# Optimization experiments

Measured on AMD Instinct MI355X. Metric: run time of the kernel, lower is better.

## Reference

```python
import jax, jax.numpy as jnp
import numpy as np

B, N, K = 16, 8192, 16
H1, H3 = 512, 64
EPS = 1e-5


def _bn(x, g, b):
    # BatchNorm1d training-mode math: normalize per-channel (last axis) over all other axes.
    ax = tuple(range(x.ndim - 1))
    m = x.mean(ax, keepdims=True)
    v = x.var(ax, keepdims=True)  # biased variance, as in torch BN forward
    return (x - m) * jax.lax.rsqrt(v + EPS) * g + b


def _gather(h, idx):
    # h: [b,n,f], idx: [b,n,k] -> [b,n,k,f] per-batch neighbor gather
    return jax.vmap(lambda hb, ib: hb[ib])(h, idx)


def _forward(data, knn, e1_w, e1_b, e1_g, e1_be,
             gc1_w, gc1_b, g1_g, g1_be, gc2_w, gc2_b, g2_g, g2_be,
             e2_w, e2_b, e2_g, e2_be,
             d1_w, d1_b, d1_g, d1_be, d2_w, d2_b, d2_g, d2_be):
    b, n, _ = data.shape
    # local covariance features
    neigh = _gather(data, knn)                       # [b,n,K,3]
    cen = neigh - neigh.mean(axis=2, keepdims=True)
    cov = jnp.einsum('bnki,bnkj->bnij', cen, cen) / (K - 1)
    x = jnp.concatenate([data, cov.reshape(b, n, 9)], axis=-1)  # [b,n,12]
    # e_layers1: Linear(12,h3) + BN + ReLU
    x = jax.nn.relu(_bn(x @ e1_w + e1_b, e1_g, e1_be))
    # GCNConv over uniform-degree kNN graph with self loop: (h_i + sum_j h_j)/(K+1)
    deg = float(K + 1)
    h = x @ gc1_w
    h = (h + _gather(h, knn).sum(axis=2)) / deg + gc1_b
    x = jax.nn.relu(_bn(h, g1_g, g1_be))
    h = x @ gc2_w
    h = (h + _gather(h, knn).sum(axis=2)) / deg + gc2_b
    x = jax.nn.relu(_bn(h, g2_g, g2_be))             # [b,n,h1]
    # AdaptiveMaxPool1d(1) over nodes
    x = x.max(axis=1, keepdims=True)                 # [b,1,h1]
    # e_layers2: Linear(h1,h1) + BN + ReLU
    x = jax.nn.relu(_bn(x @ e2_w + e2_b, e2_g, e2_be))
    # decode: folding grid
    nx_ = int(1 + (n * 120 / 60) ** 0.5)
    ny_ = int(1 + (n * 60 / 120) ** 0.5)
    xg = jnp.linspace(1.0, 120.0, nx_)
    yg = jnp.linspace(1.0, 60.0, ny_)
    grid = jnp.stack(jnp.meshgrid(xg, yg, indexing='ij'), axis=-1).reshape(-1, 2)[:n]
    kfeat = jnp.broadcast_to(x, (b, n, x.shape[-1]))  # codeword repeated per node
    y = jnp.broadcast_to(grid[None], (b, n, 2))
    z = jnp.concatenate([kfeat, y], axis=-1)          # [b,n,h1+2]
    z = jax.nn.relu(_bn(z @ d1_w + d1_b, d1_g, d1_be))
    z = jnp.concatenate([kfeat, z], axis=-1)          # [b,n,h1+3]
    z = jax.nn.relu(_bn(z @ d2_w + d2_b, d2_g, d2_be))
    return z                                          # [b,n,3]


def setup_inputs() -> dict:
    key = jax.random.key(0)
    ks = jax.random.split(key, 8)

    def lin(k, i, o):
        s = 1.0 / np.sqrt(i)
        return jax.random.uniform(k, (i, o), jnp.float32, -s, s)

    ones = lambda c: jnp.ones((c,), jnp.float32)
    zeros = lambda c: jnp.zeros((c,), jnp.float32)
    return {
        'data': jax.random.normal(ks[0], (B, N, 3), jnp.float32),
        'knn': jax.random.randint(ks[1], (B, N, K), 0, N),
        'e1_w': lin(ks[2], 12, H3), 'e1_b': zeros(H3), 'e1_g': ones(H3), 'e1_be': zeros(H3),
        'gc1_w': lin(ks[3], H3, 2 * H3), 'gc1_b': zeros(2 * H3), 'g1_g': ones(2 * H3), 'g1_be': zeros(2 * H3),
        'gc2_w': lin(ks[4], 2 * H3, H1), 'gc2_b': zeros(H1), 'g2_g': ones(H1), 'g2_be': zeros(H1),
        'e2_w': lin(ks[5], H1, H1), 'e2_b': zeros(H1), 'e2_g': ones(H1), 'e2_be': zeros(H1),
        'd1_w': lin(ks[6], H1 + 2, 3), 'd1_b': zeros(3), 'd1_g': ones(3), 'd1_be': zeros(3),
        'd2_w': lin(ks[7], H1 + 3, 3), 'd2_b': zeros(3), 'd2_g': ones(3), 'd2_be': zeros(3),
    }


def reference(data, knn, e1_w, e1_b, e1_g, e1_be,
              gc1_w, gc1_b, g1_g, g1_be, gc2_w, gc2_b, g2_g, g2_be,
              e2_w, e2_b, e2_g, e2_be,
              d1_w, d1_b, d1_g, d1_be, d2_w, d2_b, d2_g, d2_be):
    return _forward(data, knn, e1_w, e1_b, e1_g, e1_be,
                    gc1_w, gc1_b, g1_g, g1_be, gc2_w, gc2_b, g2_g, g2_be,
                    e2_w, e2_b, e2_g, e2_be,
                    d1_w, d1_b, d1_g, d1_be, d2_w, d2_b, d2_g, d2_be)
```

## Files before the change

### kernel.cpp

```cpp
#include <hip/hip_runtime.h>
#include <hip/hip_fp16.h>
#include <stdint.h>

#define BATCH 16
#define NPTS  8192
#define KNN   16
#define NROWS (BATCH*NPTS)
#define EPSBN 1e-5f
#define DEGINV (1.0f/17.0f)

typedef _Float16 f16x8 __attribute__((ext_vector_type(8)));
typedef float    f32x4 __attribute__((ext_vector_type(4)));

__device__ __forceinline__ unsigned short f2hu(float f) {
    union { _Float16 h; unsigned short u; } cv;
    cv.h = (_Float16)f;
    return cv.u;
}
__device__ __forceinline__ float hu2f(unsigned short u) {
    union { unsigned short u; _Float16 h; } cv;
    cv.u = u;
    return (float)cv.h;
}
__device__ __forceinline__ unsigned fenc(float f) {
    unsigned u = __float_as_uint(f);
    return (int)u >= 0 ? (u | 0x80000000u) : ~u;
}
__device__ __forceinline__ float fdec(unsigned k) {
    return (k & 0x80000000u) ? __uint_as_float(k & 0x7FFFFFFFu) : __uint_as_float(~k);
}

#define SZ_S1    0
#define SZ_S2P   128
#define SZ_S3P   16512
#define SZ_S4    82048
#define SZ_C1    83072
#define SZ_GN    83080
#define SZ_D2    83088
#define SZ_SCSH1 83096
#define SZ_SCSH2 83224
#define SZ_TOT   83480

__global__ __launch_bounds__(256) void k_prep(
    const float* __restrict__ gc1w, const float* __restrict__ gc2w,
    const float* __restrict__ d1w, const float* __restrict__ d1b,
    unsigned short* __restrict__ W1T, unsigned short* __restrict__ W2T,
    float* __restrict__ gn, float* __restrict__ statszone, unsigned* __restrict__ mm)
{
    int t = blockIdx.x * 256 + threadIdx.x;
    int NT_ = gridDim.x * 256;
    for (int i = t; i < 65536; i += NT_) {
        int c = i >> 7, k = i & 127;
        W2T[i] = f2hu(gc2w[k * 512 + c]);
    }
    for (int i = t; i < 8192; i += NT_) {
        int c = i >> 6, k = i & 63;
        W1T[i] = f2hu(gc1w[k * 128 + c]);
    }
    for (int i = t; i < SZ_TOT; i += NT_) statszone[i] = 0.f;
    for (int i = t; i < 8192; i += NT_) mm[i] = 0u;
    for (int i = t; i < 8192; i += NT_) mm[8192 + i] = 0xFFFFFFFFu;
    for (int n = t; n < 8192; n += NT_) {
        int ix = n / 65, iy = n % 65;
        float gx = 1.f + ix * (119.f / 128.f);
        float gy = 1.f + iy * (59.f / 64.f);
        #pragma unroll
        for (int j = 0; j < 3; j++)
            gn[n * 3 + j] = gx * d1w[512 * 3 + j] + gy * d1w[513 * 3 + j] + d1b[j];
    }
}

__global__ __launch_bounds__(256) void k_cov_e1(
    const float* __restrict__ data, const int* __restrict__ knn,
    const float* __restrict__ e1w, const float* __restrict__ e1b,
    unsigned short* __restrict__ a1)
{
    __shared__ float w[12 * 64];
    __shared__ float bias[64];
    int tid = threadIdx.x;
    for (int i = tid; i < 768; i += 256) w[i] = e1w[i];
    if (tid < 64) bias[tid] = e1b[tid];
    __syncthreads();

    int gid = blockIdx.x * 256 + tid;
    int b = gid >> 13;
    const float* db = data + (size_t)b * NPTS * 3;
    const int4* k4 = (const int4*)knn + gid * 4;

    float sx = 0, sy = 0, sz = 0, Sxx = 0, Sxy = 0, Sxz = 0, Syy = 0, Syz = 0, Szz = 0;
    #pragma unroll
    for (int jj = 0; jj < 4; jj++) {
        int4 q = k4[jj];
        int id[4] = {q.x, q.y, q.z, q.w};
        #pragma unroll
        for (int u = 0; u < 4; u++) {
            const float* p = db + (size_t)id[u] * 3;
            float x = p[0], y = p[1], z = p[2];
            sx += x; sy += y; sz += z;
            Sxx += x * x; Sxy += x * y; Sxz += x * z;
            Syy += y * y; Syz += y * z; Szz += z * z;
        }
    }
    float mx = sx * (1.f / 16.f), my = sy * (1.f / 16.f), mz = sz * (1.f / 16.f);
    const float inv15 = 1.f / 15.f;
    float x12[12];
    x12[0] = data[(size_t)gid * 3 + 0];
    x12[1] = data[(size_t)gid * 3 + 1];
    x12[2] = data[(size_t)gid * 3 + 2];
    x12[3] = (Sxx - 16.f * mx * mx) * inv15;
    x12[4] = (Sxy - 16.f * mx * my) * inv15;
    x12[5] = (Sxz - 16.f * mx * mz) * inv15;
    x12[6] = x12[4];
    x12[7] = (Syy - 16.f * my * my) * inv15;
    x12[8] = (Syz - 16.f * my * mz) * inv15;
    x12[9] = x12[5];
    x12[10] = x12[8];
    x12[11] = (Szz - 16.f * mz * mz) * inv15;

    unsigned short* arow = a1 + (size_t)gid * 64;
    for (int c0 = 0; c0 < 64; c0 += 8) {
        float v8[8];
        #pragma unroll
        for (int u = 0; u < 8; u++) {
            int c = c0 + u;
            float acc = bias[c];
            #pragma unroll
            for (int i = 0; i < 12; i++) acc += x12[i] * w[i * 64 + c];
            v8[u] = acc;
        }
        uint4 o;
        o.x = f2hu(v8[0]) | ((unsigned)f2hu(v8[1]) << 16);
        o.y = f2hu(v8[2]) | ((unsigned)f2hu(v8[3]) << 16);
        o.z = f2hu(v8[4]) | ((unsigned)f2hu(v8[5]) << 16);
        o.w = f2hu(v8[6]) | ((unsigned)f2hu(v8[7]) << 16);
        *(uint4*)(arow + c0) = o;
    }
}

__global__ __launch_bounds__(256) void k_reduce_a1(
    const unsigned short* __restrict__ a1, float* __restrict__ stats1)
{
    int tid = threadIdx.x;
    int c = tid & 63, rq = tid >> 6;
    float s = 0.f, q = 0.f;
    for (int row = blockIdx.x * 4 + rq; row < NROWS; row += gridDim.x * 4) {
        float v = hu2f(a1[(size_t)row * 64 + c]);
        s += v; q += v * v;
    }
    __shared__ float red[2][256];
    red[0][tid] = s; red[1][tid] = q;
    __syncthreads();
    if (tid < 64) {
        s = red[0][tid] + red[0][tid + 64] + red[0][tid + 128] + red[0][tid + 192];
        q = red[1][tid] + red[1][tid + 64] + red[1][tid + 128] + red[1][tid + 192];
        atomicAdd(stats1 + tid, s);
        atomicAdd(stats1 + 64 + tid, q);
    }
}

template <int C, int NPARTS>
__global__ __launch_bounds__(256) void k_bncoef(
    const float* __restrict__ statsIn,
    const float* __restrict__ gamma, const float* __restrict__ beta,
    float* __restrict__ scsh)
{
    int ch = threadIdx.x;
    if (ch < C) {
        float s = 0.f, q = 0.f;
        for (int p = 0; p < NPARTS; p++) {
            s += statsIn[p * 2 * C + ch];
            q += statsIn[p * 2 * C + C + ch];
        }
        float m = s * (1.f / NROWS);
        float var = fmaxf(q * (1.f / NROWS) - m * m, 0.f);
        float sc = gamma[ch] * rsqrtf(var + EPSBN);
        scsh[ch] = sc;
        scsh[C + ch] = beta[ch] - m * sc;
    }
}

template <int CIN>
__global__ __launch_bounds__(256) void k_gather16(
    const unsigned short* __restrict__ ain, const int* __restrict__ knn,
    const float* __restrict__ scsh, unsigned short* __restrict__ S)
{
    constexpr int GPR = CIN / 8;
    constexpr int R = 256 / GPR;
    constexpr int BPB = NPTS / R;

    __shared__ int nidx[R * KNN];

    int tid = threadIdx.x;
    int blk = blockIdx.x;
    int xcd = blk & 7;
    int idx = blk >> 3;
    int batch = xcd + 8 * (idx / BPB);
    int within = idx % BPB;
    int node0 = batch * NPTS + within * R;

    if (tid < R * KNN / 4) {
        const int4* ksrc = (const int4*)(knn + (size_t)node0 * KNN);
        ((int4*)nidx)[tid] = ksrc[tid];
    }
    __syncthreads();

    int t = tid & (GPR - 1);
    int r = tid / GPR;
    int col8 = t * 8;
    float sc8[8], sh8[8];
    #pragma unroll
    for (int j = 0; j < 8; j++) { sc8[j] = scsh[col8 + j]; sh8[j] = scsh[CIN + col8 + j]; }

    int row = node0 + r;
    const unsigned short* abase = ain + (size_t)batch * NPTS * CIN;

    float acc8[8];
    {
        uint4 v = *(const uint4*)(ain + (size_t)row * CIN + col8);
        unsigned wds[4] = {v.x, v.y, v.z, v.w};
        #pragma unroll
        for (int j = 0; j < 4; j++) {
            acc8[2*j]   = fmaxf(hu2f((unsigned short)(wds[j] & 0xFFFF)) * sc8[2*j]   + sh8[2*j],   0.f);
            acc8[2*j+1] = fmaxf(hu2f((unsigned short)(wds[j] >> 16))    * sc8[2*j+1] + sh8[2*j+1], 0.f);
        }
    }
    #pragma unroll
    for (int jn = 0; jn < KNN; jn++) {
        int src = nidx[r * KNN + jn];
        uint4 v = *(const uint4*)(abase + (size_t)src * CIN + col8);
        unsigned wds[4] = {v.x, v.y, v.z, v.w};
        #pragma unroll
        for (int j = 0; j < 4; j++) {
            acc8[2*j]   += fmaxf(hu2f((unsigned short)(wds[j] & 0xFFFF)) * sc8[2*j]   + sh8[2*j],   0.f);
            acc8[2*j+1] += fmaxf(hu2f((unsigned short)(wds[j] >> 16))    * sc8[2*j+1] + sh8[2*j+1], 0.f);
        }
    }
    uint4 o;
    o.x = f2hu(acc8[0]) | ((unsigned)f2hu(acc8[1]) << 16);
    o.y = f2hu(acc8[2]) | ((unsigned)f2hu(acc8[3]) << 16);
    o.z = f2hu(acc8[4]) | ((unsigned)f2hu(acc8[5]) << 16);
    o.w = f2hu(acc8[6]) | ((unsigned)f2hu(acc8[7]) << 16);
    *(uint4*)(S + (size_t)row * CIN + col8) = o;
}

template <int CIN, int COUT, int NSPLIT, bool STORE>
__global__ __launch_bounds__(256) void k_gemm(
    const unsigned short* __restrict__ S, const unsigned short* __restrict__ WT,
    const float* __restrict__ bias,
    unsigned short* __restrict__ aout, float* __restrict__ statsOut, unsigned* __restrict__ mm)
{
    constexpr int KC = CIN / 32;
    constexpr int MT = 128;
    constexpr int SST = CIN + 8;
    constexpr int CPB = COUT / NSPLIT;
    constexpr int CPW = CPB / 4;
    constexpr int NT = CPW / 16;

    __shared__ alignas(16) unsigned short sA[MT * SST];

    int tid = threadIdx.x;
    int blk = blockIdx.x;
    int xcd = blk & 7;
    int rest = blk >> 3;
    int nq = rest % NSPLIT;
    int mseq = rest / NSPLIT;
    int phase = mseq >> 6;
    int within = mseq & 63;
    int batch = xcd + 8 * phase;
    int node0 = batch * NPTS + within * MT;
    int cbase = nq * CPB;
    int pout = batch * 4 + (within >> 4);

    {
        constexpr int TOT = MT * CIN / 8;
        const uint4* src = (const uint4*)(S + (size_t)node0 * CIN);
        #pragma unroll
        for (int i = tid; i < TOT; i += 256) {
            int row = i / (CIN / 8);
            int col8 = (i % (CIN / 8)) * 8;
            *(uint4*)&sA[row * SST + col8] = src[i];
        }
    }
    __syncthreads();

    int lane = tid & 63, wv = tid >> 6;
    int n15 = lane & 15, qd = lane >> 4;
    int c0 = cbase + wv * CPW;

    f16x8 wf[KC][NT];
    float bz[NT];
    #pragma unroll
    for (int nt = 0; nt < NT; nt++) {
        int c = c0 + nt * 16 + n15;
        bz[nt] = bias[c];
        #pragma unroll
        for (int kc = 0; kc < KC; kc++)
            wf[kc][nt] = *(const f16x8*)(WT + (size_t)c * CIN + kc * 32 + qd * 8);
    }
    float sacc[NT], qacc[NT], mxa[NT], mna[NT];
    #pragma unroll
    for (int nt = 0; nt < NT; nt++) {
        sacc[nt] = 0.f; qacc[nt] = 0.f; mxa[nt] = -3.4e38f; mna[nt] = 3.4e38f;
    }

    #pragma unroll
    for (int mt = 0; mt < MT / 16; mt++) {
        f16x8 af[KC];
        #pragma unroll
        for (int kc = 0; kc < KC; kc++)
            af[kc] = *(const f16x8*)&sA[(mt * 16 + n15) * SST + kc * 32 + qd * 8];

        f32x4 acc[NT];
        #pragma unroll
        for (int nt = 0; nt < NT; nt++) acc[nt] = (f32x4)(0.f);
        #pragma unroll
        for (int kc = 0; kc < KC; kc++)
            #pragma unroll
            for (int nt = 0; nt < NT; nt++)
                acc[nt] = __builtin_amdgcn_mfma_f32_16x16x32_f16(af[kc], wf[kc][nt], acc[nt], 0, 0, 0);

        #pragma unroll
        for (int nt = 0; nt < NT; nt++) {
            int c = c0 + nt * 16 + n15;
            #pragma unroll
            for (int r = 0; r < 4; r++) {
                float a = acc[nt][r];
                sacc[nt] += a;
                qacc[nt] = fmaf(a, a, qacc[nt]);
                if (!STORE) {
                    mxa[nt] = fmaxf(mxa[nt], a);
                    mna[nt] = fminf(mna[nt], a);
                }
                if (STORE) {
                    float v = a * DEGINV + bz[nt];
                    int node = node0 + mt * 16 + qd * 4 + r;
                    aout[(size_t)node * COUT + c] = f2hu(v);
                }
            }
        }
    }

    #pragma unroll
    for (int nt = 0; nt < NT; nt++) {
        int c = c0 + nt * 16 + n15;
        float S_ = sacc[nt], Q_ = qacc[nt];
        S_ += __shfl_xor(S_, 16); S_ += __shfl_xor(S_, 32);
        Q_ += __shfl_xor(Q_, 16); Q_ += __shfl_xor(Q_, 32);
        if (!STORE) {
            float mx = mxa[nt], mn = mna[nt];
            mx = fmaxf(mx, __shfl_xor(mx, 16)); mx = fmaxf(mx, __shfl_xor(mx, 32));
            mn = fminf(mn, __shfl_xor(mn, 16)); mn = fminf(mn, __shfl_xor(mn, 32));
            if (lane < 16) {
                atomicMax(mm + batch * COUT + c, fenc(mx * DEGINV + bz[nt]));
                atomicMin(mm + BATCH * COUT + batch * COUT + c, fenc(mn * DEGINV + bz[nt]));
            }
        }
        if (lane < 16) {
            float b = bz[nt];
            float s = DEGINV * S_ + (float)MT * b;
            float q = DEGINV * DEGINV * Q_ + 2.f * DEGINV * b * S_ + (float)MT * b * b;
            atomicAdd(statsOut + (size_t)pout * 2 * COUT + c, s);
            atomicAdd(statsOut + (size_t)pout * 2 * COUT + COUT + c, q);
        }
    }
}

__global__ __launch_bounds__(256) void k_e2(
    const float* __restrict__ stats3p, const unsigned* __restrict__ mm,
    const float* __restrict__ g2g, const float* __restrict__ g2be,
    const float* __restrict__ e2w, const float* __restrict__ e2b,
    float* __restrict__ a4, float* __restrict__ stats4)
{
    __shared__ float pooled[512];
    int b = blockIdx.x, tid = threadIdx.x;
    for (int c = tid; c < 512; c += 256) {
        float s = 0.f, qq = 0.f;
        for (int p = 0; p < 64; p++) {
            s += stats3p[p * 1024 + c];
            qq += stats3p[p * 1024 + 512 + c];
        }
        float m = s * (1.f / NROWS);
        float var = fmaxf(qq * (1.f / NROWS) - m * m, 0.f);
        float sc = g2g[c] * rsqrtf(var + EPSBN);
        float sh = g2be[c] - m * sc;
        float amax = fdec(mm[b * 512 + c]);
        float amin = fdec(mm[8192 + b * 512 + c]);
        pooled[c] = fmaxf(fmaxf(sc * amax + sh, 0.f), fmaxf(sc * amin + sh, 0.f));
    }
    __syncthreads();
    int ca = tid, cb = tid + 256;
    float acc1 = e2b[ca], acc2 = e2b[cb];
    for (int f = 0; f < 512; f++) {
        float pv = pooled[f];
        acc1 += pv * e2w[f * 512 + ca];
        acc2 += pv * e2w[f * 512 + cb];
    }
    a4[b * 512 + ca] = acc1; a4[b * 512 + cb] = acc2;
    atomicAdd(stats4 + ca, acc1); atomicAdd(stats4 + 512 + ca, acc1 * acc1);
    atomicAdd(stats4 + cb, acc2); atomicAdd(stats4 + 512 + cb, acc2 * acc2);
}

__global__ __launch_bounds__(256) void k_code(
    const float* __restrict__ a4, const float* __restrict__ stats4,
    const float* __restrict__ e2g, const float* __restrict__ e2be,
    const float* __restrict__ d1w, const float* __restrict__ d2w,
    const float* __restrict__ gn,
    float* __restrict__ c1, float* __restrict__ c2,
    float* __restrict__ c1stats, float* __restrict__ gnstats)
{
    int b = blockIdx.x, tid = threadIdx.x;
    int lane = tid & 63, wv = tid >> 6;
    float p1[3] = {0, 0, 0}, p2[3] = {0, 0, 0};
    for (int c = tid; c < 512; c += 256) {
        float s = stats4[c], qq = stats4[512 + c];
        float m = s * (1.f / 16.f);
        float var = fmaxf(qq * (1.f / 16.f) - m * m, 0.f);
        float sc = e2g[c] * rsqrtf(var + EPSBN);
        float sh = e2be[c] - m * sc;
        float cv = fmaxf(sc * a4[b * 512 + c] + sh, 0.f);
        #pragma unroll
        for (int j = 0; j < 3; j++) {
            p1[j] += cv * d1w[c * 3 + j];
            p2[j] += cv * d2w[c * 3 + j];
        }
    }
    __shared__ float red[4][6];
    #pragma unroll
    for (int j = 0; j < 3; j++)
        for (int off = 32; off; off >>= 1) {
            p1[j] += __shfl_xor(p1[j], off);
            p2[j] += __shfl_xor(p2[j], off);
        }
    if (lane == 0) {
        #pragma unroll
        for (int j = 0; j < 3; j++) { red[wv][j] = p1[j]; red[wv][3 + j] = p2[j]; }
    }
    __syncthreads();
    if (tid < 3) {
        float v = red[0][tid] + red[1][tid] + red[2][tid] + red[3][tid];
        c1[b * 3 + tid] = v;
        atomicAdd(c1stats + tid, v);
        atomicAdd(c1stats + 3 + tid, v * v);
    } else if (tid < 6) {
        int j = tid - 3;
        float v = red[0][tid] + red[1][tid] + red[2][tid] + red[3][tid];
        c2[b * 3 + j] = v;
    }
    if (blockIdx.x == 0) {
        float g1[3] = {0, 0, 0}, g2s[3] = {0, 0, 0};
        for (int n = tid; n < NPTS; n += 256) {
            #pragma unroll
            for (int j = 0; j < 3; j++) {
                float g = gn[n * 3 + j];
                g1[j] += g; g2s[j] += g * g;
            }
        }
        #pragma unroll
        for (int j = 0; j < 3; j++)
            for (int off = 32; off; off >>= 1) {
                g1[j] += __shfl_xor(g1[j], off);
                g2s[j] += __shfl_xor(g2s[j], off);
            }
        __shared__ float redg[4][6];
        if (lane == 0) {
            #pragma unroll
            for (int j = 0; j < 3; j++) { redg[wv][j] = g1[j]; redg[wv][3 + j] = g2s[j]; }
        }
        __syncthreads();
        if (tid < 6)
            gnstats[tid] = redg[0][tid] + redg[1][tid] + redg[2][tid] + redg[3][tid];
    }
}

__device__ __forceinline__ void d1_coefs(
    const float* c1stats, const float* gnstats,
    const float* d1g, const float* d1be, float* scd, float* shd)
{
    #pragma unroll
    for (int j = 0; j < 3; j++) {
        float mc = c1stats[j] * (1.f / 16.f), qc = c1stats[3 + j] * (1.f / 16.f);
        float mg = gnstats[j] * (1.f / 8192.f), qg = gnstats[3 + j] * (1.f / 8192.f);
        float m = mc + mg;
        float var = fmaxf((qc - mc * mc) + (qg - mg * mg), 0.f);
        float sc = d1g[j] * rsqrtf(var + EPSBN);
        scd[j] = sc;
        shd[j] = d1be[j] - m * sc;
    }
}

__global__ __launch_bounds__(256) void k_d2stats(
    const float* __restrict__ c1, const float* __restrict__ c2, const float* __restrict__ gn,
    const float* __restrict__ c1stats, const float* __restrict__ gnstats,
    const float* __restrict__ d1g, const float* __restrict__ d1be,
    const float* __restrict__ d2w, const float* __restrict__ d2b,
    float* __restrict__ statsd2)
{
    int gid = blockIdx.x * 256 + threadIdx.x;
    int b = gid >> 13, n = gid & 8191;
    int lane = threadIdx.x & 63, wv = threadIdx.x >> 6;
    float scd[3], shd[3];
    d1_coefs(c1stats, gnstats, d1g, d1be, scd, shd);
    float z3[3];
    #pragma unroll
    for (int j = 0; j < 3; j++)
        z3[j] = fmaxf(scd[j] * (c1[b * 3 + j] + gn[n * 3 + j]) + shd[j], 0.f);
    float vals[6];
    #pragma unroll
    for (int u = 0; u < 3; u++) {
        float a = c2[b * 3 + u]
                + z3[0] * d2w[512 * 3 + u]
                + z3[1] * d2w[513 * 3 + u]
                + z3[2] * d2w[514 * 3 + u]
                + d2b[u];
        vals[u] = a; vals[3 + u] = a * a;
    }
    #pragma unroll
    for (int j = 0; j < 6; j++)
        for (int off = 32; off; off >>= 1) vals[j] += __shfl_xor(vals[j], off);
    __shared__ float red[4][6];
    if (lane == 0) {
        #pragma unroll
        for (int j = 0; j < 6; j++) red[wv][j] = vals[j];
    }
    __syncthreads();
    if (threadIdx.x < 6)
        atomicAdd(statsd2 + threadIdx.x,
                  red[0][threadIdx.x] + red[1][threadIdx.x] + red[2][threadIdx.x] + red[3][threadIdx.x]);
}

__global__ __launch_bounds__(256) void k_out(
    const float* __restrict__ c1, const float* __restrict__ c2, const float* __restrict__ gn,
    const float* __restrict__ c1stats, const float* __restrict__ gnstats,
    const float* __restrict__ statsd2,
    const float* __restrict__ d1g, const float* __restrict__ d1be,
    const float* __restrict__ d2w, const float* __restrict__ d2b,
    const float* __restrict__ d2g, const float* __restrict__ d2be,
    float* __restrict__ out)
{
    int gid = blockIdx.x * 256 + threadIdx.x;
    int b = gid >> 13, n = gid & 8191;
    float scd[3], shd[3];
    d1_coefs(c1stats, gnstats, d1g, d1be, scd, shd);
    float z3[3];
    #pragma unroll
    for (int j = 0; j < 3; j++)
        z3[j] = fmaxf(scd[j] * (c1[b * 3 + j] + gn[n * 3 + j]) + shd[j], 0.f);
    #pragma unroll
    for (int u = 0; u < 3; u++) {
        float a = c2[b * 3 + u]
                + z3[0] * d2w[512 * 3 + u]
                + z3[1] * d2w[513 * 3 + u]
                + z3[2] * d2w[514 * 3 + u]
                + d2b[u];
        float m2 = statsd2[u] * (1.f / (float)NROWS);
        float v2 = fmaxf(statsd2[3 + u] * (1.f / (float)NROWS) - m2 * m2, 0.f);
        float sc = d2g[u] * rsqrtf(v2 + EPSBN);
        float sh = d2be[u] - m2 * sc;
        out[(size_t)gid * 3 + u] = fmaxf(sc * a + sh, 0.f);
    }
}

extern "C" void kernel_launch(void* const* d_in, const int* in_sizes, int n_in,
                              void* d_out, int out_size, void* d_ws, size_t ws_size,
                              hipStream_t stream)
{
    (void)in_sizes; (void)n_in; (void)out_size; (void)ws_size;
    const float* data = (const float*)d_in[0];
    const int*   knn  = (const int*)d_in[1];
    const float* e1w = (const float*)d_in[2],  *e1b = (const float*)d_in[3];
    const float* e1g = (const float*)d_in[4],  *e1be = (const float*)d_in[5];
    const float* gc1w = (const float*)d_in[6], *gc1b = (const float*)d_in[7];
    const float* g1g = (const float*)d_in[8],  *g1be = (const float*)d_in[9];
    const float* gc2w = (const float*)d_in[10], *gc2b = (const float*)d_in[11];
    const float* g2g = (const float*)d_in[12], *g2be = (const float*)d_in[13];
    const float* e2w = (const float*)d_in[14], *e2b = (const float*)d_in[15];
    const float* e2g = (const float*)d_in[16], *e2be = (const float*)d_in[17];
    const float* d1w = (const float*)d_in[18], *d1b = (const float*)d_in[19];
    const float* d1g = (const float*)d_in[20], *d1be = (const float*)d_in[21];
    const float* d2w = (const float*)d_in[22], *d2b = (const float*)d_in[23];
    const float* d2g = (const float*)d_in[24], *d2be = (const float*)d_in[25];

    char* p = (char*)d_ws;
    auto alloc = [&](size_t bytes) -> void* {
        void* r = (void*)p;
        p += (bytes + 255) & ~(size_t)255;
        return r;
    };
    unsigned short* a1  = (unsigned short*)alloc((size_t)NROWS * 64 * 2);
    unsigned short* a2h = (unsigned short*)alloc((size_t)NROWS * 128 * 2);
    unsigned short* s1  = (unsigned short*)alloc((size_t)NROWS * 64 * 2);
    unsigned short* s2  = (unsigned short*)alloc((size_t)NROWS * 128 * 2);
    unsigned short* W1T = (unsigned short*)alloc(8192 * 2);
    unsigned short* W2T = (unsigned short*)alloc(65536 * 2);
    float* statszone = (float*)alloc(SZ_TOT * 4);
    float* stats1  = statszone + SZ_S1;
    float* stats2p = statszone + SZ_S2P;
    float* stats3p = statszone + SZ_S3P;
    float* stats4  = statszone + SZ_S4;
    float* c1stats = statszone + SZ_C1;
    float* gnstats = statszone + SZ_GN;
    float* statsd2 = statszone + SZ_D2;
    float* scsh1   = statszone + SZ_SCSH1;
    float* scsh2   = statszone + SZ_SCSH2;
    unsigned* mm = (unsigned*)alloc(16384 * 4);
    float* a4 = (float*)alloc(16 * 512 * 4);
    float* c1 = (float*)alloc(64 * 4);
    float* c2 = (float*)alloc(64 * 4);
    float* gn = (float*)alloc(8192 * 3 * 4);

    k_prep<<<64, 256, 0, stream>>>(gc1w, gc2w, d1w, d1b, W1T, W2T, gn, statszone, mm);
    k_cov_e1<<<512, 256, 0, stream>>>(data, knn, e1w, e1b, a1);
    k_reduce_a1<<<256, 256, 0, stream>>>(a1, stats1);
    k_bncoef<64, 1><<<1, 256, 0, stream>>>(stats1, e1g, e1be, scsh1);
    k_gather16<64><<<NROWS / 32, 256, 0, stream>>>(a1, knn, scsh1, s1);
    k_gemm<64, 128, 1, true><<<1024, 256, 0, stream>>>(s1, W1T, gc1b, a2h, stats2p, nullptr);
    k_bncoef<128, 64><<<1, 256, 0, stream>>>(stats2p, g1g, g1be, scsh2);
    k_gather16<128><<<NROWS / 16, 256, 0, stream>>>(a2h, knn, scsh2, s2);
    k_gemm<128, 512, 4, false><<<4096, 256, 0, stream>>>(s2, W2T, gc2b, nullptr, stats3p, mm);
    k_e2<<<16, 256, 0, stream>>>(stats3p, mm, g2g, g2be, e2w, e2b, a4, stats4);
    k_code<<<16, 256, 0, stream>>>(a4, stats4, e2g, e2be, d1w, d2w, gn, c1, c2, c1stats, gnstats);
    k_d2stats<<<512, 256, 0, stream>>>(c1, c2, gn, c1stats, gnstats, d1g, d1be, d2w, d2b, statsd2);
    k_out<<<512, 256, 0, stream>>>(c1, c2, gn, c1stats, gnstats, statsd2,
                                   d1g, d1be, d2w, d2b, d2g, d2be, (float*)d_out);
}
```

Measured before the change: 334.9 us.

## Fuse BN1 stats into cov kernel and process two rows per gather thread

Computes the first BatchNorm's sum and sum-of-squares inside k_cov_e1 via wavefront shuffle reductions and atomics into 8 partial slots, which removes the separate k_reduce_a1 pass that re-read a1. The gather kernels now handle two node rows per thread, halving the grid size and putting two independent neighbor loads in flight per iteration. In exchange, the cov kernel does more work, issues more atomics to a small set of addresses, and the gather threads use more registers.

```diff
diff --git a/kernel.cpp b/kernel.cpp
--- a/kernel.cpp
+++ b/kernel.cpp
@@ -31,15 +31,15 @@
 }
 
 #define SZ_S1    0
-#define SZ_S2P   128
-#define SZ_S3P   16512
-#define SZ_S4    82048
-#define SZ_C1    83072
-#define SZ_GN    83080
-#define SZ_D2    83088
-#define SZ_SCSH1 83096
-#define SZ_SCSH2 83224
-#define SZ_TOT   83480
+#define SZ_S2P   1024
+#define SZ_S3P   17408
+#define SZ_S4    82944
+#define SZ_C1    83968
+#define SZ_GN    83976
+#define SZ_D2    83984
+#define SZ_SCSH1 83992
+#define SZ_SCSH2 84120
+#define SZ_TOT   84376
 
 __global__ __launch_bounds__(256) void k_prep(
     const float* __restrict__ gc1w, const float* __restrict__ gc2w,
@@ -73,7 +73,7 @@
 __global__ __launch_bounds__(256) void k_cov_e1(
     const float* __restrict__ data, const int* __restrict__ knn,
     const float* __restrict__ e1w, const float* __restrict__ e1b,
-    unsigned short* __restrict__ a1)
+    unsigned short* __restrict__ a1, float* __restrict__ stats1)
 {
     __shared__ float w[12 * 64];
     __shared__ float bias[64];
@@ -84,6 +84,8 @@
 
     int gid = blockIdx.x * 256 + tid;
     int b = gid >> 13;
+    int lane = tid & 63;
+    int pout = blockIdx.x & 7;
     const float* db = data + (size_t)b * NPTS * 3;
     const int4* k4 = (const int4*)knn + gid * 4;
 
@@ -134,27 +136,19 @@
         o.z = f2hu(v8[4]) | ((unsigned)f2hu(v8[5]) << 16);
         o.w = f2hu(v8[6]) | ((unsigned)f2hu(v8[7]) << 16);
         *(uint4*)(arow + c0) = o;
-    }
-}
-
-__global__ __launch_bounds__(256) void k_reduce_a1(
-    const unsigned short* __restrict__ a1, float* __restrict__ stats1)
-{
-    int tid = threadIdx.x;
-    int c = tid & 63, rq = tid >> 6;
-    float s = 0.f, q = 0.f;
-    for (int row = blockIdx.x * 4 + rq; row < NROWS; row += gridDim.x * 4) {
-        float v = hu2f(a1[(size_t)row * 64 + c]);
-        s += v; q += v * v;
-    }
-    __shared__ float red[2][256];
-    red[0][tid] = s; red[1][tid] = q;
-    __syncthreads();
-    if (tid < 64) {
-        s = red[0][tid] + red[0][tid + 64] + red[0][tid + 128] + red[0][tid + 192];
-        q = red[1][tid] + red[1][tid + 64] + red[1][tid + 128] + red[1][tid + 192];
-        atomicAdd(stats1 + tid, s);
-        atomicAdd(stats1 + 64 + tid, q);
+        #pragma unroll
+        for (int u = 0; u < 8; u++) {
+            float s = v8[u], q = v8[u] * v8[u];
+            #pragma unroll
+            for (int off = 1; off < 64; off <<= 1) {
+                s += __shfl_xor(s, off);
+                q += __shfl_xor(q, off);
+            }
+            if (lane == 0) {
+                atomicAdd(stats1 + pout * 128 + c0 + u, s);
+                atomicAdd(stats1 + pout * 128 + 64 + c0 + u, q);
+            }
+        }
     }
 }
 
@@ -186,9 +180,10 @@
 {
     constexpr int GPR = CIN / 8;
     constexpr int R = 256 / GPR;
-    constexpr int BPB = NPTS / R;
-
-    __shared__ int nidx[R * KNN];
+    constexpr int R2 = 2 * R;
+    constexpr int BPB = NPTS / R2;
+
+    __shared__ int nidx[R2 * KNN];
 
     int tid = threadIdx.x;
     int blk = blockIdx.x;
@@ -196,51 +191,66 @@
     int idx = blk >> 3;
     int batch = xcd + 8 * (idx / BPB);
     int within = idx % BPB;
-    int node0 = batch * NPTS + within * R;
-
-    if (tid < R * KNN / 4) {
+    int node0 = batch * NPTS + within * R2;
+
+    {
         const int4* ksrc = (const int4*)(knn + (size_t)node0 * KNN);
-        ((int4*)nidx)[tid] = ksrc[tid];
+        for (int i = tid; i < R2 * 4; i += 256) ((int4*)nidx)[i] = ksrc[i];
     }
     __syncthreads();
 
     int t = tid & (GPR - 1);
-    int r = tid / GPR;
+    int r0 = tid / GPR;
     int col8 = t * 8;
     float sc8[8], sh8[8];
     #pragma unroll
     for (int j = 0; j < 8; j++) { sc8[j] = scsh[col8 + j]; sh8[j] = scsh[CIN + col8 + j]; }
 
-    int row = node0 + r;
+    int ra = node0 + r0;
+    int rb = node0 + r0 + R;
     const unsigned short* abase = ain + (size_t)batch * NPTS * CIN;
 
-    float acc8[8];
+    float acca[8], accb[8];
     {
-        uint4 v = *(const uint4*)(ain + (size_t)row * CIN + col8);
-        unsigned wds[4] = {v.x, v.y, v.z, v.w};
+        uint4 va = *(const uint4*)(ain + (size_t)ra * CIN + col8);
+        uint4 vb = *(const uint4*)(ain + (size_t)rb * CIN + col8);
+        unsigned wa[4] = {va.x, va.y, va.z, va.w};
+        unsigned wb[4] = {vb.x, vb.y, vb.z, vb.w};
         #pragma unroll
         for (int j = 0; j < 4; j++) {
-            acc8[2*j]   = fmaxf(hu2f((unsigned short)(wds[j] & 0xFFFF)) * sc8[2*j]   + sh8[2*j],   0.f);
-            acc8[2*j+1] = fmaxf(hu2f((unsigned short)(wds[j] >> 16))    * sc8[2*j+1] + sh8[2*j+1], 0.f);
+            acca[2*j]   = fmaxf(hu2f((unsigned short)(wa[j] & 0xFFFF)) * sc8[2*j]   + sh8[2*j],   0.f);
+            acca[2*j+1] = fmaxf(hu2f((unsigned short)(wa[j] >> 16))    * sc8[2*j+1] + sh8[2*j+1], 0.f);
+            accb[2*j]   = fmaxf(hu2f((unsigned short)(wb[j] & 0xFFFF)) * sc8[2*j]   + sh8[2*j],   0.f);
+            accb[2*j+1] = fmaxf(hu2f((unsigned short)(wb[j] >> 16))    * sc8[2*j+1] + sh8[2*j+1], 0.f);
         }
     }
     #pragma unroll
     for (int jn = 0; jn < KNN; jn++) {
-        int src = nidx[r * KNN + jn];
-        uint4 v = *(const uint4*)(abase + (size_t)src * CIN + col8);
-        unsigned wds[4] = {v.x, v.y, v.z, v.w};
+        int sa = nidx[r0 * KNN + jn];
+        int sb = nidx[(r0 + R) * KNN + jn];
+        uint4 va = *(const uint4*)(abase + (size_t)sa * CIN + col8);
+        uint4 vb = *(const uint4*)(abase + (size_t)sb * CIN + col8);
+        unsigned wa[4] = {va.x, va.y, va.z, va.w};
+        unsigned wb[4] = {vb.x, vb.y, vb.z, vb.w};
         #pragma unroll
         for (int j = 0; j < 4; j++) {
-            acc8[2*j]   += fmaxf(hu2f((unsigned short)(wds[j] & 0xFFFF)) * sc8[2*j]   + sh8[2*j],   0.f);
-            acc8[2*j+1] += fmaxf(hu2f((unsigned short)(wds[j] >> 16))    * sc8[2*j+1] + sh8[2*j+1], 0.f);
-        }
-    }
-    uint4 o;
-    o.x = f2hu(acc8[0]) | ((unsigned)f2hu(acc8[1]) << 16);
-    o.y = f2hu(acc8[2]) | ((unsigned)f2hu(acc8[3]) << 16);
-    o.z = f2hu(acc8[4]) | ((unsigned)f2hu(acc8[5]) << 16);
-    o.w = f2hu(acc8[6]) | ((unsigned)f2hu(acc8[7]) << 16);
-    *(uint4*)(S + (size_t)row * CIN + col8) = o;
+            acca[2*j]   += fmaxf(hu2f((unsigned short)(wa[j] & 0xFFFF)) * sc8[2*j]   + sh8[2*j],   0.f);
+            acca[2*j+1] += fmaxf(hu2f((unsigned short)(wa[j] >> 16))    * sc8[2*j+1] + sh8[2*j+1], 0.f);
+            accb[2*j]   += fmaxf(hu2f((unsigned short)(wb[j] & 0xFFFF)) * sc8[2*j]   + sh8[2*j],   0.f);
+            accb[2*j+1] += fmaxf(hu2f((unsigned short)(wb[j] >> 16))    * sc8[2*j+1] + sh8[2*j+1], 0.f);
+        }
+    }
+    uint4 oa, ob;
+    oa.x = f2hu(acca[0]) | ((unsigned)f2hu(acca[1]) << 16);
+    oa.y = f2hu(acca[2]) | ((unsigned)f2hu(acca[3]) << 16);
+    oa.z = f2hu(acca[4]) | ((unsigned)f2hu(acca[5]) << 16);
+    oa.w = f2hu(acca[6]) | ((unsigned)f2hu(acca[7]) << 16);
+    ob.x = f2hu(accb[0]) | ((unsigned)f2hu(accb[1]) << 16);
+    ob.y = f2hu(accb[2]) | ((unsigned)f2hu(accb[3]) << 16);
+    ob.z = f2hu(accb[4]) | ((unsigned)f2hu(accb[5]) << 16);
+    ob.w = f2hu(accb[6]) | ((unsigned)f2hu(accb[7]) << 16);
+    *(uint4*)(S + (size_t)ra * CIN + col8) = oa;
+    *(uint4*)(S + (size_t)rb * CIN + col8) = ob;
 }
 
 template <int CIN, int COUT, int NSPLIT, bool STORE>
@@ -609,13 +619,12 @@
     float* gn = (float*)alloc(8192 * 3 * 4);
 
     k_prep<<<64, 256, 0, stream>>>(gc1w, gc2w, d1w, d1b, W1T, W2T, gn, statszone, mm);
-    k_cov_e1<<<512, 256, 0, stream>>>(data, knn, e1w, e1b, a1);
-    k_reduce_a1<<<256, 256, 0, stream>>>(a1, stats1);
-    k_bncoef<64, 1><<<1, 256, 0, stream>>>(stats1, e1g, e1be, scsh1);
-    k_gather16<64><<<NROWS / 32, 256, 0, stream>>>(a1, knn, scsh1, s1);
+    k_cov_e1<<<512, 256, 0, stream>>>(data, knn, e1w, e1b, a1, stats1);
+    k_bncoef<64, 8><<<1, 256, 0, stream>>>(stats1, e1g, e1be, scsh1);
+    k_gather16<64><<<NROWS / 64, 256, 0, stream>>>(a1, knn, scsh1, s1);
     k_gemm<64, 128, 1, true><<<1024, 256, 0, stream>>>(s1, W1T, gc1b, a2h, stats2p, nullptr);
     k_bncoef<128, 64><<<1, 256, 0, stream>>>(stats2p, g1g, g1be, scsh2);
-    k_gather16<128><<<NROWS / 16, 256, 0, stream>>>(a2h, knn, scsh2, s2);
+    k_gather16<128><<<NROWS / 32, 256, 0, stream>>>(a2h, knn, scsh2, s2);
     k_gemm<128, 512, 4, false><<<4096, 256, 0, stream>>>(s2, W2T, gc2b, nullptr, stats3p, mm);
     k_e2<<<16, 256, 0, stream>>>(stats3p, mm, g2g, g2be, e2w, e2b, a4, stats4);
     k_code<<<16, 256, 0, stream>>>(a4, stats4, e2g, e2be, d1w, d2w, gn, c1, c2, c1stats, gnstats);
```

Result: slower. 425.1 us (+26.9%).
